# Kernel tuning notes

Hardware: AMD Instinct MI355X
Metric: run time of the kernel (lower is better)

The kernel has to match this reference:

```python
import jax, jax.numpy as jnp
import numpy as np

HEADS = 16
HEAD_DIM = 64
LN_EPS = 1e-5


def setup_inputs() -> dict:
    key = jax.random.key(0)
    k_x, k_q, k_k, k_v = jax.random.split(key, 4)
    B, C, H, W = 32, 640, 32, 32
    inner = HEADS * HEAD_DIM  # 1024
    x = jax.random.normal(k_x, (B, C, H, W), dtype=jnp.float32)
    # nn.Linear(in_dim, inner_dim, bias=False): weight shape [inner, in_dim]
    Wq = jax.random.normal(k_q, (inner, C), dtype=jnp.float32) * 0.02
    Wk = jax.random.normal(k_k, (inner, C), dtype=jnp.float32) * 0.02
    Wv = jax.random.normal(k_v, (inner, C), dtype=jnp.float32) * 0.02
    # out_norm = nn.LayerNorm(head_dim): default init gamma=1, beta=0
    gamma = jnp.ones((HEAD_DIM,), dtype=jnp.float32)
    beta = jnp.zeros((HEAD_DIM,), dtype=jnp.float32)
    return {"x": x, "Wq": Wq, "Wk": Wk, "Wv": Wv, "gamma": gamma, "beta": beta}


def _layernorm(y, gamma, beta):
    mu = jnp.mean(y, axis=-1, keepdims=True)
    var = jnp.mean(jnp.square(y - mu), axis=-1, keepdims=True)
    return (y - mu) * jax.lax.rsqrt(var + LN_EPS) * gamma + beta


def reference(x, Wq, Wk, Wv, gamma, beta):
    B, C, H, W = x.shape
    N = H * W
    scale = HEAD_DIM ** -0.5
    # rearrange 'b c h w -> b (h w) c' (patch_size=1)
    t = x.reshape(B, C, N).transpose(0, 2, 1)  # [B, N, C]
    def proj(Wm):
        p = jnp.einsum('bnc,ec->bne', t, Wm)  # [B, N, inner]
        return p.reshape(B, N, HEADS, HEAD_DIM).transpose(0, 2, 1, 3)  # [B, h, N, d]
    q, k, v = proj(Wq), proj(Wk), proj(Wv)
    qk = jnp.einsum('bhid,bhjd->bhij', q, k)  # [B, h, N, N]
    p_att = jax.nn.softmax(qk * scale, axis=-1)
    out = jnp.einsum('bhij,bhjd->bhid', p_att, v)  # [B, h, N, d]
    out = out.mean(axis=2)  # [B, h, d]
    return _layernorm(out, gamma, beta)
```

## Files before the change

### kernel.cpp

```cpp
#include <hip/hip_runtime.h>
#include <hip/hip_bf16.h>

typedef __bf16 bf16;
typedef __bf16 bf16x8 __attribute__((ext_vector_type(8)));
typedef float f32x4 __attribute__((ext_vector_type(4)));

#define QSCALE 0.18033688011112042f

#define EXP2(x) __builtin_amdgcn_exp2f(x)

__device__ __forceinline__ void load_lds16(const void* gp, void* lp) {
  __builtin_amdgcn_global_load_lds((const __attribute__((address_space(1))) void*)gp,
                                   (__attribute__((address_space(3))) void*)lp, 16, 0, 0);
}

__global__ __launch_bounds__(256) void k_transpose(const float* __restrict__ x,
                                                   bf16* __restrict__ t) {
  __shared__ float tile[64][65];
  const int b = blockIdx.z, c0 = blockIdx.y * 64, n0 = blockIdx.x * 64;
  const int tid = threadIdx.x, lx = tid & 63, ly = tid >> 6;
  const float* xp = x + ((size_t)b * 640 + c0) * 1024 + n0;
#pragma unroll
  for (int i = 0; i < 16; ++i) {
    int c = i * 4 + ly;
    tile[c][lx] = xp[(size_t)c * 1024 + lx];
  }
  __syncthreads();
  bf16* tp = t + ((size_t)b * 1024 + n0) * 640 + c0;
#pragma unroll
  for (int i = 0; i < 16; ++i) {
    int n = i * 4 + ly;
    tp[(size_t)n * 640 + lx] = (bf16)tile[lx][n];
  }
}

__global__ __launch_bounds__(256) void k_castw(const float* __restrict__ w,
                                               bf16* __restrict__ dst, float s) {
  int i = blockIdx.x * 256 + threadIdx.x;
  if (i < 655360) dst[i] = (bf16)(w[i] * s);
}

__global__ __launch_bounds__(256) void k_gemm_qkv(const bf16* __restrict__ A,
                                                  const bf16* __restrict__ Bw,
                                                  bf16* __restrict__ qkv) {
  __shared__ __align__(16) bf16 As[128 * 64];
  __shared__ __align__(16) bf16 Bs[128 * 64];
  const int tid = threadIdx.x;
  const int lane = tid & 63;
  const int w = tid >> 6;
  const int wm = w & 1, wn = w >> 1;
  const int g = lane >> 4, ln = lane & 15;
  const int m0 = blockIdx.x * 128;
  const int n0 = blockIdx.y * 128;

  f32x4 acc[4][4];
#pragma unroll
  for (int i = 0; i < 4; ++i)
#pragma unroll
    for (int j = 0; j < 4; ++j)
#pragma unroll
      for (int r = 0; r < 4; ++r) acc[i][j][r] = 0.f;

  for (int k0 = 0; k0 < 640; k0 += 64) {
#pragma unroll
    for (int it = 0; it < 4; ++it) {
      int c = it * 256 + w * 64 + lane;
      int m = c >> 3;
      int kq = (c & 7) ^ (m & 7);
      load_lds16(A + (size_t)(m0 + m) * 640 + (k0 + kq * 8), As + (size_t)(it * 256 + w * 64) * 8);
      load_lds16(Bw + (size_t)(n0 + m) * 640 + (k0 + kq * 8), Bs + (size_t)(it * 256 + w * 64) * 8);
    }
    __syncthreads();
#pragma unroll
    for (int kk = 0; kk < 2; ++kk) {
      bf16x8 af[4], bfr[4];
#pragma unroll
      for (int mi = 0; mi < 4; ++mi) {
        int m = wm * 64 + mi * 16 + ln;
        int cc = m * 8 + ((kk * 4 + g) ^ (m & 7));
        af[mi] = *(const bf16x8*)(As + cc * 8);
      }
#pragma unroll
      for (int ni = 0; ni < 4; ++ni) {
        int n = wn * 64 + ni * 16 + ln;
        int cc = n * 8 + ((kk * 4 + g) ^ (n & 7));
        bfr[ni] = *(const bf16x8*)(Bs + cc * 8);
      }
#pragma unroll
      for (int mi = 0; mi < 4; ++mi)
#pragma unroll
        for (int ni = 0; ni < 4; ++ni)
          acc[mi][ni] = __builtin_amdgcn_mfma_f32_16x16x32_bf16(af[mi], bfr[ni], acc[mi][ni], 0, 0, 0);
    }
    __syncthreads();
  }

#pragma unroll
  for (int mi = 0; mi < 4; ++mi)
#pragma unroll
    for (int ni = 0; ni < 4; ++ni)
#pragma unroll
      for (int r = 0; r < 4; ++r) {
        int row = m0 + wm * 64 + mi * 16 + g * 4 + r;
        int col = n0 + wn * 64 + ni * 16 + ln;
        int bb = row >> 10, n = row & 1023;
        int which = col >> 10, h = (col >> 6) & 15, d = col & 63;
        qkv[(size_t)which * 33554432 +
            ((((size_t)bb * 16 + h) * 1024 + n) * 64 + d)] = (bf16)acc[mi][ni][r];
      }
}

__global__ __launch_bounds__(256) void k_attn(const bf16* __restrict__ q,
                                              const bf16* __restrict__ kmat,
                                              float* __restrict__ wsum) {
  const int idx = blockIdx.x;
  const int xcd = idx & 7;
  const int y = idx >> 3;
  const int it = y & 3;
  const int bh = xcd + ((y >> 2) << 3);
  const int tid = threadIdx.x;
  const int lane = tid & 63;
  const int w = tid >> 6;
  const int g = lane >> 4, ln = lane & 15;
  const bf16* qb = q + (size_t)bh * 65536;
  const bf16* kb = kmat + (size_t)bh * 65536;
  const int i0 = it * 256 + w * 64;

  const f32x4 zf = {0.f, 0.f, 0.f, 0.f};

  bf16x8 qf[4][2];
#pragma unroll
  for (int mi = 0; mi < 4; ++mi)
#pragma unroll
    for (int kc = 0; kc < 2; ++kc)
      qf[mi][kc] = *(const bf16x8*)(qb + (size_t)(i0 + mi * 16 + ln) * 64 + kc * 32 + g * 8);

  float rs[4][4];
#pragma unroll
  for (int mi = 0; mi < 4; ++mi)
#pragma unroll
    for (int r = 0; r < 4; ++r) rs[mi][r] = 0.f;

  for (int jt = 0; jt < 16; ++jt) {
    bf16x8 kf[4][2];
#pragma unroll
    for (int ni = 0; ni < 4; ++ni)
#pragma unroll
      for (int kc = 0; kc < 2; ++kc)
        kf[ni][kc] = *(const bf16x8*)(kb + (size_t)(jt * 64 + ni * 16 + ln) * 64 + kc * 32 + g * 8);
#pragma unroll
    for (int mi = 0; mi < 4; ++mi)
#pragma unroll
      for (int ni = 0; ni < 4; ++ni) {
        f32x4 s = __builtin_amdgcn_mfma_f32_16x16x32_bf16(qf[mi][0], kf[ni][0], zf, 0, 0, 0);
        s = __builtin_amdgcn_mfma_f32_16x16x32_bf16(qf[mi][1], kf[ni][1], s, 0, 0, 0);
#pragma unroll
        for (int r = 0; r < 4; ++r) rs[mi][r] += EXP2(s[r]);
      }
  }
  float rinv[4][4];
#pragma unroll
  for (int mi = 0; mi < 4; ++mi)
#pragma unroll
    for (int r = 0; r < 4; ++r) {
      float v = rs[mi][r];
      v += __shfl_xor(v, 1);
      v += __shfl_xor(v, 2);
      v += __shfl_xor(v, 4);
      v += __shfl_xor(v, 8);
      rinv[mi][r] = 1.0f / v;
    }

  for (int jt = 0; jt < 16; ++jt) {
    bf16x8 kf[4][2];
#pragma unroll
    for (int ni = 0; ni < 4; ++ni)
#pragma unroll
      for (int kc = 0; kc < 2; ++kc)
        kf[ni][kc] = *(const bf16x8*)(kb + (size_t)(jt * 64 + ni * 16 + ln) * 64 + kc * 32 + g * 8);
    float cs[4] = {0.f, 0.f, 0.f, 0.f};
#pragma unroll
    for (int mi = 0; mi < 4; ++mi)
#pragma unroll
      for (int ni = 0; ni < 4; ++ni) {
        f32x4 s = __builtin_amdgcn_mfma_f32_16x16x32_bf16(qf[mi][0], kf[ni][0], zf, 0, 0, 0);
        s = __builtin_amdgcn_mfma_f32_16x16x32_bf16(qf[mi][1], kf[ni][1], s, 0, 0, 0);
#pragma unroll
        for (int r = 0; r < 4; ++r) cs[ni] += EXP2(s[r]) * rinv[mi][r];
      }
#pragma unroll
    for (int ni = 0; ni < 4; ++ni) {
      float v = cs[ni];
      v += __shfl_xor(v, 16);
      v += __shfl_xor(v, 32);
      if (g == 0) atomicAdd(wsum + (size_t)bh * 1024 + jt * 64 + ni * 16 + ln, v);
    }
  }
}

__global__ __launch_bounds__(256) void k_final(const float* __restrict__ wsum,
                                               const bf16* __restrict__ v,
                                               const float* __restrict__ gamma,
                                               const float* __restrict__ beta,
                                               float* __restrict__ out) {
  const int bh = blockIdx.x;
  const int tid = threadIdx.x;
  const int d = tid & 63, part = tid >> 6;
  const bf16* vb = v + (size_t)bh * 65536;
  const float* wb = wsum + (size_t)bh * 1024;
  float acc = 0.f;
  for (int j = part * 256; j < part * 256 + 256; ++j)
    acc += wb[j] * (float)vb[(size_t)j * 64 + d];
  __shared__ float red[4][64];
  red[part][d] = acc;
  __syncthreads();
  if (tid < 64) {
    float y = (red[0][d] + red[1][d] + red[2][d] + red[3][d]) * (1.0f / 1024.0f);
    float s1 = y;
#pragma unroll
    for (int off = 1; off < 64; off <<= 1) s1 += __shfl_xor(s1, off);
    float mu = s1 * (1.0f / 64.0f);
    float dy = y - mu;
    float s2 = dy * dy;
#pragma unroll
    for (int off = 1; off < 64; off <<= 1) s2 += __shfl_xor(s2, off);
    float rstd = rsqrtf(s2 * (1.0f / 64.0f) + 1e-5f);
    out[(size_t)bh * 64 + d] = dy * rstd * gamma[d] + beta[d];
  }
}

extern "C" void kernel_launch(void* const* d_in, const int* in_sizes, int n_in,
                              void* d_out, int out_size, void* d_ws, size_t ws_size,
                              hipStream_t stream) {
  const float* x     = (const float*)d_in[0];
  const float* Wq    = (const float*)d_in[1];
  const float* Wk    = (const float*)d_in[2];
  const float* Wv    = (const float*)d_in[3];
  const float* gamma = (const float*)d_in[4];
  const float* beta  = (const float*)d_in[5];
  float* out = (float*)d_out;

  char* ws = (char*)d_ws;
  bf16*  tbf  = (bf16*)ws;
  bf16*  wbf  = (bf16*)(ws + 41943040);
  bf16*  qkv  = (bf16*)(ws + 45875200);
  float* wsum = (float*)(ws + 247201792);

  hipMemsetAsync(wsum, 0, (size_t)512 * 1024 * sizeof(float), stream);
  k_transpose<<<dim3(16, 10, 32), 256, 0, stream>>>(x, tbf);
  k_castw<<<2560, 256, 0, stream>>>(Wq, wbf, QSCALE);
  k_castw<<<2560, 256, 0, stream>>>(Wk, wbf + 655360, 1.0f);
  k_castw<<<2560, 256, 0, stream>>>(Wv, wbf + 1310720, 1.0f);
  k_gemm_qkv<<<dim3(256, 24), 256, 0, stream>>>(tbf, wbf, qkv);
  k_attn<<<2048, 256, 0, stream>>>(qkv, qkv + 33554432, wsum);
  k_final<<<512, 256, 0, stream>>>(wsum, qkv + 67108864, gamma, beta, out);
}
```

Measured before the change: 566.4 us.

## Stage K tiles in swizzled, double-buffered LDS shared across waves in attention

The attention kernel now copies each 64-row K tile once per block into LDS with direct global-to-LDS loads, double-buffered, with an XOR swizzle to avoid bank conflicts. Before, each of the four waves loaded its K fragments from global memory separately. This cuts redundant global/L2 traffic by about four times and overlaps the next tile's load with compute. The cost is a block-wide barrier every tile and reliance on the async LDS loads having completed before the barrier.

```diff
diff --git a/kernel.cpp b/kernel.cpp
--- a/kernel.cpp
+++ b/kernel.cpp
@@ -113,6 +113,7 @@
 __global__ __launch_bounds__(256) void k_attn(const bf16* __restrict__ q,
                                               const bf16* __restrict__ kmat,
                                               float* __restrict__ wsum) {
+  __shared__ __align__(16) bf16 Ks[2][4096];
   const int idx = blockIdx.x;
   const int xcd = idx & 7;
   const int y = idx >> 3;
@@ -128,6 +129,21 @@
 
   const f32x4 zf = {0.f, 0.f, 0.f, 0.f};
 
+#define STAGEK(buf, jt)                                                       \
+  do {                                                                        \
+    _Pragma("unroll") for (int call_ = 0; call_ < 2; ++call_) {               \
+      int p_ = w * 128 + call_ * 64 + lane;                                   \
+      int j_ = p_ >> 3;                                                       \
+      int kq_ = (p_ & 7) ^ (j_ & 7);                                          \
+      load_lds16(kb + (size_t)((jt) * 64 + j_) * 64 + kq_ * 8,                \
+                 &Ks[buf][(size_t)(w * 128 + call_ * 64) * 8]);               \
+    }                                                                         \
+  } while (0)
+
+#define KFRAG(buf, ni, kc)                                                    \
+  (*(const bf16x8*)(&Ks[buf][(size_t)(((ni) * 16 + ln) * 8 +                  \
+                                      (((kc) * 4 + g) ^ (ln & 7))) * 8]))
+
   bf16x8 qf[4][2];
 #pragma unroll
   for (int mi = 0; mi < 4; ++mi)
@@ -141,13 +157,16 @@
 #pragma unroll
     for (int r = 0; r < 4; ++r) rs[mi][r] = 0.f;
 
+  STAGEK(0, 0);
   for (int jt = 0; jt < 16; ++jt) {
+    const int cur = jt & 1;
+    __syncthreads();
+    if (jt + 1 < 16) STAGEK(1 - cur, jt + 1);
     bf16x8 kf[4][2];
 #pragma unroll
     for (int ni = 0; ni < 4; ++ni)
 #pragma unroll
-      for (int kc = 0; kc < 2; ++kc)
-        kf[ni][kc] = *(const bf16x8*)(kb + (size_t)(jt * 64 + ni * 16 + ln) * 64 + kc * 32 + g * 8);
+      for (int kc = 0; kc < 2; ++kc) kf[ni][kc] = KFRAG(cur, ni, kc);
 #pragma unroll
     for (int mi = 0; mi < 4; ++mi)
 #pragma unroll
@@ -171,13 +190,16 @@
       rinv[mi][r] = 1.0f / v;
     }
 
+  STAGEK(0, 0);
   for (int jt = 0; jt < 16; ++jt) {
+    const int cur = jt & 1;
+    __syncthreads();
+    if (jt + 1 < 16) STAGEK(1 - cur, jt + 1);
     bf16x8 kf[4][2];
 #pragma unroll
     for (int ni = 0; ni < 4; ++ni)
 #pragma unroll
-      for (int kc = 0; kc < 2; ++kc)
-        kf[ni][kc] = *(const bf16x8*)(kb + (size_t)(jt * 64 + ni * 16 + ln) * 64 + kc * 32 + g * 8);
+      for (int kc = 0; kc < 2; ++kc) kf[ni][kc] = KFRAG(cur, ni, kc);
     float cs[4] = {0.f, 0.f, 0.f, 0.f};
 #pragma unroll
     for (int mi = 0; mi < 4; ++mi)
@@ -196,6 +218,8 @@
       if (g == 0) atomicAdd(wsum + (size_t)bh * 1024 + jt * 64 + ni * 16 + ln, v);
     }
   }
+#undef STAGEK
+#undef KFRAG
 }
 
 __global__ __launch_bounds__(256) void k_final(const float* __restrict__ wsum,
```

After: 518.4 us. 1.09x faster.
